# Optimization experiments

Measured on AMD Instinct MI355X. Metric: run time of the kernel, lower is better.

The kernel has to match this reference:

```python
import jax, jax.numpy as jnp
import numpy as np

B, CIN, D, H, W = 2, 64, 16, 16, 16
CK, CV, COUT = 32, 64, 64
EPS = 1e-5


def setup_inputs() -> dict:
    key = jax.random.key(0)
    ks = jax.random.split(key, 11)
    return {
        "x": jax.random.normal(ks[0], (B, CIN, D, H, W), jnp.float32),
        "key_w": jax.random.normal(ks[1], (CK, CIN), jnp.float32) * 0.1,
        "bn_gamma": jax.random.uniform(ks[2], (CK,), jnp.float32, 0.5, 1.5),
        "bn_beta": jax.random.normal(ks[3], (CK,), jnp.float32) * 0.1,
        "bn_mean": jax.random.normal(ks[4], (CK,), jnp.float32) * 0.1,
        "bn_var": jax.random.uniform(ks[5], (CK,), jnp.float32, 0.5, 1.5),
        "value_w": jax.random.normal(ks[6], (CV, CIN), jnp.float32) * 0.1,
        "value_b": jax.random.normal(ks[7], (CV,), jnp.float32) * 0.1,
        "W_w": jax.random.normal(ks[8], (COUT, CV), jnp.float32) * 0.1,
        "W_b": jax.random.normal(ks[9], (COUT,), jnp.float32) * 0.1,
        "gamma": jax.random.normal(ks[10], (1,), jnp.float32),
    }


def reference(x, key_w, bn_gamma, bn_beta, bn_mean, bn_var,
              value_w, value_b, W_w, W_b, gamma):
    b, c, d, h, w = x.shape
    n = d * h * w
    xf = x.reshape(b, c, n)                       # [B, Cin, N]
    # f_key: 1x1x1 conv (no bias) + BatchNorm3d (eval mode, running stats)
    k = jnp.einsum('oc,bcn->bon', key_w, xf)      # [B, Ck, N]
    scale_bn = bn_gamma / jnp.sqrt(bn_var + EPS)
    k = (k - bn_mean[:, None]) * scale_bn[:, None] + bn_beta[:, None]
    # key_query_same=True -> query == key (same weights, same input)
    # f_value: 1x1x1 conv with bias
    v = jnp.einsum('oc,bcn->bon', value_w, xf) + value_b[:, None]  # [B, Cv, N]
    # sim_map = Q^T K scaled, softmax over last axis
    sim = jnp.einsum('bkn,bkm->bnm', k, k) * (CK ** -0.5)          # [B, N, N]
    sim = jax.nn.softmax(sim, axis=-1)
    # context = sim @ V^T  -> [B, N, Cv] -> [B, Cv, N]
    ctx = jnp.einsum('bnm,bvm->bvn', sim, v)
    # W: 1x1x1 conv
    ctx = jnp.einsum('ov,bvn->bon', W_w, ctx) + W_b[:, None]       # [B, Cout, N]
    ctx = ctx.reshape(b, COUT, d, h, w)
    # out_add=True branch: gamma * context + x
    return gamma.reshape(()) * ctx + x
```

## Files before the change

### kernel.cpp

```cpp
#include <hip/hip_runtime.h>
#include <hip/hip_bf16.h>
#include <math.h>

#define BATCH 2
#define CIN 64
#define NSP 4096
#define CK 32
#define CV 64
#define COUT 64
#define EPS 1e-5f
#define S4L 0.5050097680523077f

#define KB 64
#define NW 8
#define KPW (NSP / NW)
#define NCH (KPW / KB)

typedef unsigned short ushort_t;
using bf16x8 = __attribute__((ext_vector_type(8))) short;
using bf16x4 = __attribute__((ext_vector_type(4))) short;
using f32x4  = __attribute__((ext_vector_type(4))) float;
using float4_t = __attribute__((ext_vector_type(4))) float;

__device__ inline ushort_t f2bf(float f) {
  __hip_bfloat16 h = __float2bfloat16(f);
  return *reinterpret_cast<ushort_t*>(&h);
}

__global__ __launch_bounds__(256) void kv_kernel(
    const float* __restrict__ x,
    const float* __restrict__ key_w,
    const float* __restrict__ bn_gamma,
    const float* __restrict__ bn_beta,
    const float* __restrict__ bn_mean,
    const float* __restrict__ bn_var,
    const float* __restrict__ value_w,
    const float* __restrict__ value_b,
    ushort_t* __restrict__ KbT,
    ushort_t* __restrict__ Vbf) {
  __shared__ ushort_t XL[32][66];

  int tid = threadIdx.x, wid = tid >> 6, lane = tid & 63;
  int l15 = lane & 15, g = lane >> 4;
  int b  = blockIdx.x / (NSP / 32);
  int n0 = (blockIdx.x % (NSP / 32)) * 32;

  {
    int n = tid & 31, c8 = tid >> 5;
    const float* xb = x + ((size_t)b * CIN + c8 * 8) * NSP + n0 + n;
#pragma unroll
    for (int j = 0; j < 8; ++j)
      XL[n][c8 * 8 + j] = f2bf(xb[(size_t)j * NSP]);
  }
  __syncthreads();

  if (wid < 2) {
    bf16x8 a[2];
#pragma unroll
    for (int kk = 0; kk < 2; ++kk)
      a[kk] = *(const bf16x8*)&XL[wid * 16 + l15][kk * 32 + g * 8];
#pragma unroll
    for (int osub = 0; osub < 2; ++osub) {
      bf16x8 bb[2];
#pragma unroll
      for (int kk = 0; kk < 2; ++kk) {
        const float* wp = key_w + (osub * 16 + l15) * CIN + kk * 32 + g * 8;
#pragma unroll
        for (int j = 0; j < 8; ++j) bb[kk][j] = (short)f2bf(wp[j]);
      }
      f32x4 d = {0.f, 0.f, 0.f, 0.f};
      d = __builtin_amdgcn_mfma_f32_16x16x32_bf16(a[0], bb[0], d, 0, 0, 0);
      d = __builtin_amdgcn_mfma_f32_16x16x32_bf16(a[1], bb[1], d, 0, 0, 0);
      int o = osub * 16 + l15;
      float sc  = bn_gamma[o] * rsqrtf(bn_var[o] + EPS);
      float scl = sc * S4L;
      float bi  = (bn_beta[o] - bn_mean[o] * sc) * S4L;
#pragma unroll
      for (int r = 0; r < 4; ++r) {
        int n = n0 + wid * 16 + 4 * g + r;
        KbT[((size_t)b * NSP + n) * CK + o] = f2bf(d[r] * scl + bi);
      }
    }
  } else {
    bf16x8 bbv[2][2];
#pragma unroll
    for (int nsub = 0; nsub < 2; ++nsub)
#pragma unroll
      for (int kk = 0; kk < 2; ++kk)
        bbv[nsub][kk] = *(const bf16x8*)&XL[nsub * 16 + l15][kk * 32 + g * 8];
#pragma unroll
    for (int os = 0; os < 2; ++os) {
      int osub = (wid - 2) * 2 + os;
      bf16x8 av[2];
#pragma unroll
      for (int kk = 0; kk < 2; ++kk) {
        const float* wp = value_w + (osub * 16 + l15) * CIN + kk * 32 + g * 8;
#pragma unroll
        for (int j = 0; j < 8; ++j) av[kk][j] = (short)f2bf(wp[j]);
      }
#pragma unroll
      for (int nsub = 0; nsub < 2; ++nsub) {
        f32x4 d = {0.f, 0.f, 0.f, 0.f};
        d = __builtin_amdgcn_mfma_f32_16x16x32_bf16(av[0], bbv[nsub][0], d, 0, 0, 0);
        d = __builtin_amdgcn_mfma_f32_16x16x32_bf16(av[1], bbv[nsub][1], d, 0, 0, 0);
#pragma unroll
        for (int r = 0; r < 4; ++r) {
          int o = osub * 16 + 4 * g + r;
          int n = n0 + nsub * 16 + l15;
          Vbf[((size_t)b * CV + o) * NSP + n] = f2bf(d[r] + value_b[o]);
        }
      }
    }
  }
}

__global__ __launch_bounds__(512) void attn_proj_kernel(
    const ushort_t* __restrict__ KbT,
    const ushort_t* __restrict__ Vbf,
    const float* __restrict__ Ww,
    const float* __restrict__ Wb,
    const float* __restrict__ gamma,
    const float* __restrict__ x,
    float* __restrict__ out) {
  __shared__ __align__(16) ushort_t SMEM[NW * 8192];

  int tid = threadIdx.x, wid = tid >> 6, lane = tid & 63;
  int l15 = lane & 15, g = lane >> 4;
  int b  = blockIdx.x / (NSP / 32);
  int q0 = (blockIdx.x % (NSP / 32)) * 32;

  const ushort_t* Kb = KbT + (size_t)b * NSP * CK;
  const ushort_t* Vb = Vbf + (size_t)b * CV * NSP;

  bf16x8 qf[2];
#pragma unroll
  for (int qg = 0; qg < 2; ++qg)
    qf[qg] = *(const bf16x8*)&Kb[(size_t)(q0 + qg * 16 + l15) * CK + g * 8];
  asm volatile("s_waitcnt vmcnt(0)" ::: "memory");
  __builtin_amdgcn_sched_barrier(0);

  f32x4 acc[2][4];
  float Ssum[2] = {0.f, 0.f};
#pragma unroll
  for (int qg = 0; qg < 2; ++qg)
#pragma unroll
    for (int cg = 0; cg < 4; ++cg)
#pragma unroll
      for (int r = 0; r < 4; ++r) acc[qg][cg][r] = 0.f;

  int kbase = wid * KPW;

  auto stageK = [&](int buf, int n0k) {
    ushort_t* dstb = &SMEM[wid * 8192 + buf * 2048];
#pragma unroll
    for (int i = 0; i < 4; ++i) {
      int off = i * 1024 + lane * 16;
      int key = off >> 6;
      int c16 = (off >> 4) & 3;
      int sw  = c16 ^ ((key >> 1) & 3);
      const ushort_t* src = Kb + (size_t)(n0k + key) * CK + sw * 8;
      __builtin_amdgcn_global_load_lds(
          (const __attribute__((address_space(1))) unsigned int*)src,
          (__attribute__((address_space(3))) unsigned int*)&dstb[i * 512], 16, 0, 0);
    }
  };
  auto stageV = [&](int n0k) {
    ushort_t* dstb = &SMEM[wid * 8192 + 4096];
#pragma unroll
    for (int i = 0; i < 8; ++i) {
      int off = i * 1024 + lane * 16;
      int cv  = off >> 7;
      int c16 = (off >> 4) & 7;
      int sw  = c16 ^ (cv & 7);
      const ushort_t* src = Vb + (size_t)cv * NSP + n0k + sw * 8;
      __builtin_amdgcn_global_load_lds(
          (const __attribute__((address_space(1))) unsigned int*)src,
          (__attribute__((address_space(3))) unsigned int*)&dstb[i * 512], 16, 0, 0);
    }
  };

  stageK(0, kbase);
  stageV(kbase);
  stageK(1, kbase + KB);
  asm volatile("s_waitcnt vmcnt(12)" ::: "memory");
  __builtin_amdgcn_sched_barrier(0);

#pragma unroll
  for (int t = 0; t < NCH; ++t) {
    const ushort_t* KTc = &SMEM[wid * 8192 + (t & 1) * 2048];
    const ushort_t* VTc = &SMEM[wid * 8192 + 4096];

    bf16x8 kf[4];
#pragma unroll
    for (int kg = 0; kg < 4; ++kg) {
      int key = kg * 16 + l15;
      int sw  = g ^ ((key >> 1) & 3);
      kf[kg] = *(const bf16x8*)&KTc[key * CK + sw * 8];
    }
    f32x4 s[2][4];
#pragma unroll
    for (int qg = 0; qg < 2; ++qg)
#pragma unroll
      for (int kg = 0; kg < 4; ++kg) {
        f32x4 z = {0.f, 0.f, 0.f, 0.f};
        s[qg][kg] = __builtin_amdgcn_mfma_f32_16x16x32_bf16(kf[kg], qf[qg], z, 0, 0, 0);
      }

    float p[2][4][4];
#pragma unroll
    for (int qg = 0; qg < 2; ++qg)
#pragma unroll
      for (int kg = 0; kg < 4; ++kg) {
        float ps = 0.f;
#pragma unroll
        for (int r = 0; r < 4; ++r) {
          p[qg][kg][r] = exp2f(s[qg][kg][r]);
          ps += p[qg][kg][r];
        }
        Ssum[qg] += ps;
      }
    bf16x8 pa[2][2];
#pragma unroll
    for (int ks = 0; ks < 2; ++ks)
#pragma unroll
      for (int qg = 0; qg < 2; ++qg)
#pragma unroll
        for (int j = 0; j < 4; ++j) {
          pa[ks][qg][j]     = (short)f2bf(p[qg][2 * ks][j]);
          pa[ks][qg][4 + j] = (short)f2bf(p[qg][2 * ks + 1][j]);
        }

    if (t < NCH - 1) asm volatile("s_waitcnt vmcnt(4)" ::: "memory");
    else             asm volatile("s_waitcnt vmcnt(0)" ::: "memory");
    __builtin_amdgcn_sched_barrier(0);

#pragma unroll
    for (int ks = 0; ks < 2; ++ks) {
#pragma unroll
      for (int cg = 0; cg < 4; ++cg) {
        int cv   = cg * 16 + l15;
        int x7   = cv & 7;
        int half = (g & 1) * 4;
        int t0   = (4 * ks + (g >> 1)) ^ x7;
        int t1   = (4 * ks + 2 + (g >> 1)) ^ x7;
        const ushort_t* vrow = &VTc[cv * KB];
        bf16x4 lo = *(const bf16x4*)&vrow[t0 * 8 + half];
        bf16x4 hi = *(const bf16x4*)&vrow[t1 * 8 + half];
        bf16x8 vf;
#pragma unroll
        for (int j = 0; j < 4; ++j) { vf[j] = lo[j]; vf[4 + j] = hi[j]; }
#pragma unroll
        for (int qg = 0; qg < 2; ++qg)
          acc[qg][cg] = __builtin_amdgcn_mfma_f32_16x16x32_bf16(pa[ks][qg], vf, acc[qg][cg], 0, 0, 0);
      }
    }

    asm volatile("s_waitcnt lgkmcnt(0)" ::: "memory");
    __builtin_amdgcn_sched_barrier(0);

    if (t + 1 < NCH) stageV(kbase + (t + 1) * KB);
    if (t + 2 < NCH) stageK(t & 1, kbase + (t + 2) * KB);

    if (t + 2 < NCH)      asm volatile("s_waitcnt vmcnt(12)" ::: "memory");
    else if (t + 1 < NCH) asm volatile("s_waitcnt vmcnt(8)" ::: "memory");
    __builtin_amdgcn_sched_barrier(0);
  }

#pragma unroll
  for (int qg = 0; qg < 2; ++qg) {
    Ssum[qg] += __shfl_xor(Ssum[qg], 16, 64);
    Ssum[qg] += __shfl_xor(Ssum[qg], 32, 64);
  }

  __syncthreads();
  float* red = (float*)&SMEM[0];
  float* SsR = red + NW * 32 * 68;
#pragma unroll
  for (int qg = 0; qg < 2; ++qg) {
#pragma unroll
    for (int cg = 0; cg < 4; ++cg)
#pragma unroll
      for (int r = 0; r < 4; ++r) {
        int ql = qg * 16 + 4 * g + r;
        red[(wid * 32 + ql) * 68 + cg * 16 + l15] = acc[qg][cg][r];
      }
    if (g == 0) SsR[wid * 32 + qg * 16 + l15] = Ssum[qg];
  }
  __syncthreads();

  int n  = tid & 31;
  int og = tid >> 5;
  float ds = 0.f;
#pragma unroll
  for (int w = 0; w < NW; ++w) ds += SsR[w * 32 + n];
  float invn = 1.f / ds;

  const float4_t* Ww4 = (const float4_t*)Ww;
  float pacc[4];
#pragma unroll
  for (int j = 0; j < 4; ++j) pacc[j] = 0.f;
#pragma unroll
  for (int v4 = 0; v4 < 16; ++v4) {
    float4_t c4 = {0.f, 0.f, 0.f, 0.f};
#pragma unroll
    for (int w = 0; w < NW; ++w) {
      float4_t t4 = *(const float4_t*)&red[(w * 32 + n) * 68 + v4 * 4];
      c4[0] += t4[0]; c4[1] += t4[1]; c4[2] += t4[2]; c4[3] += t4[3];
    }
#pragma unroll
    for (int j = 0; j < 4; ++j) {
      float4_t w4 = Ww4[(og * 4 + j) * 16 + v4];
      pacc[j] += w4[0] * c4[0] + w4[1] * c4[1] + w4[2] * c4[2] + w4[3] * c4[3];
    }
  }

  float gma = gamma[0];
#pragma unroll
  for (int j = 0; j < 4; ++j) {
    int o = og * 4 + j;
    size_t oi = ((size_t)b * COUT + o) * NSP + q0 + n;
    out[oi] = gma * (pacc[j] * invn + Wb[o]) + x[oi];
  }
}

extern "C" void kernel_launch(void* const* d_in, const int* in_sizes, int n_in,
                              void* d_out, int out_size, void* d_ws, size_t ws_size,
                              hipStream_t stream) {
  const float* x        = (const float*)d_in[0];
  const float* key_w    = (const float*)d_in[1];
  const float* bn_gamma = (const float*)d_in[2];
  const float* bn_beta  = (const float*)d_in[3];
  const float* bn_mean  = (const float*)d_in[4];
  const float* bn_var   = (const float*)d_in[5];
  const float* value_w  = (const float*)d_in[6];
  const float* value_b  = (const float*)d_in[7];
  const float* W_w      = (const float*)d_in[8];
  const float* W_b      = (const float*)d_in[9];
  const float* gamma    = (const float*)d_in[10];
  float* out = (float*)d_out;

  ushort_t* KbT = (ushort_t*)d_ws;
  ushort_t* Vbf = KbT + (size_t)BATCH * NSP * CK;

  kv_kernel<<<BATCH * (NSP / 32), 256, 0, stream>>>(
      x, key_w, bn_gamma, bn_beta, bn_mean, bn_var, value_w, value_b, KbT, Vbf);
  attn_proj_kernel<<<BATCH * (NSP / 32), 512, 0, stream>>>(
      KbT, Vbf, W_w, W_b, gamma, x, out);
}
```

Measured before the change: 30.40 us.

## Split key range across 16 waves with smaller chunks and two-level reduction

The attention kernel now runs 1024 threads (16 waves) per 32-query block instead of 8 waves, and halves the key chunk size to 32 so per-wave LDS stays the same in total. The cross-wave reduction becomes two-stage: the upper 8 waves write partials, the lower 8 add and rewrite them, and the final projection then gives each thread 2 output channels. The aim is more latency hiding and shorter per-wave serial loops. The cost is less work per async load, a smaller MFMA batch per chunk, and an extra barrier in the reduction.

```diff
diff --git a/kernel.cpp b/kernel.cpp
--- a/kernel.cpp
+++ b/kernel.cpp
@@ -11,8 +11,8 @@
 #define EPS 1e-5f
 #define S4L 0.5050097680523077f
 
-#define KB 64
-#define NW 8
+#define KB 32
+#define NW 16
 #define KPW (NSP / NW)
 #define NCH (KPW / KB)
 
@@ -114,7 +114,7 @@
   }
 }
 
-__global__ __launch_bounds__(512) void attn_proj_kernel(
+__global__ __launch_bounds__(1024, 4) void attn_proj_kernel(
     const ushort_t* __restrict__ KbT,
     const ushort_t* __restrict__ Vbf,
     const float* __restrict__ Ww,
@@ -122,7 +122,7 @@
     const float* __restrict__ gamma,
     const float* __restrict__ x,
     float* __restrict__ out) {
-  __shared__ __align__(16) ushort_t SMEM[NW * 8192];
+  __shared__ __align__(16) ushort_t SMEM[NW * 4096];
 
   int tid = threadIdx.x, wid = tid >> 6, lane = tid & 63;
   int l15 = lane & 15, g = lane >> 4;
@@ -151,9 +151,9 @@
   int kbase = wid * KPW;
 
   auto stageK = [&](int buf, int n0k) {
-    ushort_t* dstb = &SMEM[wid * 8192 + buf * 2048];
-#pragma unroll
-    for (int i = 0; i < 4; ++i) {
+    ushort_t* dstb = &SMEM[wid * 4096 + buf * 1024];
+#pragma unroll
+    for (int i = 0; i < 2; ++i) {
       int off = i * 1024 + lane * 16;
       int key = off >> 6;
       int c16 = (off >> 4) & 3;
@@ -165,13 +165,13 @@
     }
   };
   auto stageV = [&](int n0k) {
-    ushort_t* dstb = &SMEM[wid * 8192 + 4096];
-#pragma unroll
-    for (int i = 0; i < 8; ++i) {
+    ushort_t* dstb = &SMEM[wid * 4096 + 2048];
+#pragma unroll
+    for (int i = 0; i < 4; ++i) {
       int off = i * 1024 + lane * 16;
-      int cv  = off >> 7;
-      int c16 = (off >> 4) & 7;
-      int sw  = c16 ^ (cv & 7);
+      int cv  = off >> 6;
+      int c16 = (off >> 4) & 3;
+      int sw  = c16 ^ (cv & 3);
       const ushort_t* src = Vb + (size_t)cv * NSP + n0k + sw * 8;
       __builtin_amdgcn_global_load_lds(
           (const __attribute__((address_space(1))) unsigned int*)src,
@@ -182,35 +182,35 @@
   stageK(0, kbase);
   stageV(kbase);
   stageK(1, kbase + KB);
-  asm volatile("s_waitcnt vmcnt(12)" ::: "memory");
+  asm volatile("s_waitcnt vmcnt(6)" ::: "memory");
   __builtin_amdgcn_sched_barrier(0);
 
 #pragma unroll
   for (int t = 0; t < NCH; ++t) {
-    const ushort_t* KTc = &SMEM[wid * 8192 + (t & 1) * 2048];
-    const ushort_t* VTc = &SMEM[wid * 8192 + 4096];
-
-    bf16x8 kf[4];
-#pragma unroll
-    for (int kg = 0; kg < 4; ++kg) {
+    const ushort_t* KTc = &SMEM[wid * 4096 + (t & 1) * 1024];
+    const ushort_t* VTc = &SMEM[wid * 4096 + 2048];
+
+    bf16x8 kf[2];
+#pragma unroll
+    for (int kg = 0; kg < 2; ++kg) {
       int key = kg * 16 + l15;
       int sw  = g ^ ((key >> 1) & 3);
       kf[kg] = *(const bf16x8*)&KTc[key * CK + sw * 8];
     }
-    f32x4 s[2][4];
+    f32x4 s[2][2];
 #pragma unroll
     for (int qg = 0; qg < 2; ++qg)
 #pragma unroll
-      for (int kg = 0; kg < 4; ++kg) {
+      for (int kg = 0; kg < 2; ++kg) {
         f32x4 z = {0.f, 0.f, 0.f, 0.f};
         s[qg][kg] = __builtin_amdgcn_mfma_f32_16x16x32_bf16(kf[kg], qf[qg], z, 0, 0, 0);
       }
 
-    float p[2][4][4];
+    float p[2][2][4];
 #pragma unroll
     for (int qg = 0; qg < 2; ++qg)
 #pragma unroll
-      for (int kg = 0; kg < 4; ++kg) {
+      for (int kg = 0; kg < 2; ++kg) {
         float ps = 0.f;
 #pragma unroll
         for (int r = 0; r < 4; ++r) {
@@ -219,40 +219,35 @@
         }
         Ssum[qg] += ps;
       }
-    bf16x8 pa[2][2];
-#pragma unroll
-    for (int ks = 0; ks < 2; ++ks)
-#pragma unroll
-      for (int qg = 0; qg < 2; ++qg)
-#pragma unroll
-        for (int j = 0; j < 4; ++j) {
-          pa[ks][qg][j]     = (short)f2bf(p[qg][2 * ks][j]);
-          pa[ks][qg][4 + j] = (short)f2bf(p[qg][2 * ks + 1][j]);
-        }
-
-    if (t < NCH - 1) asm volatile("s_waitcnt vmcnt(4)" ::: "memory");
+    bf16x8 pa[2];
+#pragma unroll
+    for (int qg = 0; qg < 2; ++qg)
+#pragma unroll
+      for (int j = 0; j < 4; ++j) {
+        pa[qg][j]     = (short)f2bf(p[qg][0][j]);
+        pa[qg][4 + j] = (short)f2bf(p[qg][1][j]);
+      }
+
+    if (t < NCH - 1) asm volatile("s_waitcnt vmcnt(2)" ::: "memory");
     else             asm volatile("s_waitcnt vmcnt(0)" ::: "memory");
     __builtin_amdgcn_sched_barrier(0);
 
 #pragma unroll
-    for (int ks = 0; ks < 2; ++ks) {
-#pragma unroll
-      for (int cg = 0; cg < 4; ++cg) {
-        int cv   = cg * 16 + l15;
-        int x7   = cv & 7;
-        int half = (g & 1) * 4;
-        int t0   = (4 * ks + (g >> 1)) ^ x7;
-        int t1   = (4 * ks + 2 + (g >> 1)) ^ x7;
-        const ushort_t* vrow = &VTc[cv * KB];
-        bf16x4 lo = *(const bf16x4*)&vrow[t0 * 8 + half];
-        bf16x4 hi = *(const bf16x4*)&vrow[t1 * 8 + half];
-        bf16x8 vf;
-#pragma unroll
-        for (int j = 0; j < 4; ++j) { vf[j] = lo[j]; vf[4 + j] = hi[j]; }
-#pragma unroll
-        for (int qg = 0; qg < 2; ++qg)
-          acc[qg][cg] = __builtin_amdgcn_mfma_f32_16x16x32_bf16(pa[ks][qg], vf, acc[qg][cg], 0, 0, 0);
-      }
+    for (int cg = 0; cg < 4; ++cg) {
+      int cv   = cg * 16 + l15;
+      int x3   = cv & 3;
+      int half = (g & 1) * 4;
+      int t0   = (g >> 1) ^ x3;
+      int t1   = (2 + (g >> 1)) ^ x3;
+      const ushort_t* vrow = &VTc[cv * KB];
+      bf16x4 lo = *(const bf16x4*)&vrow[t0 * 8 + half];
+      bf16x4 hi = *(const bf16x4*)&vrow[t1 * 8 + half];
+      bf16x8 vf;
+#pragma unroll
+      for (int j = 0; j < 4; ++j) { vf[j] = lo[j]; vf[4 + j] = hi[j]; }
+#pragma unroll
+      for (int qg = 0; qg < 2; ++qg)
+        acc[qg][cg] = __builtin_amdgcn_mfma_f32_16x16x32_bf16(pa[qg], vf, acc[qg][cg], 0, 0, 0);
     }
 
     asm volatile("s_waitcnt lgkmcnt(0)" ::: "memory");
@@ -261,8 +256,8 @@
     if (t + 1 < NCH) stageV(kbase + (t + 1) * KB);
     if (t + 2 < NCH) stageK(t & 1, kbase + (t + 2) * KB);
 
-    if (t + 2 < NCH)      asm volatile("s_waitcnt vmcnt(12)" ::: "memory");
-    else if (t + 1 < NCH) asm volatile("s_waitcnt vmcnt(8)" ::: "memory");
+    if (t + 2 < NCH)      asm volatile("s_waitcnt vmcnt(6)" ::: "memory");
+    else if (t + 1 < NCH) asm volatile("s_waitcnt vmcnt(4)" ::: "memory");
     __builtin_amdgcn_sched_barrier(0);
   }
 
@@ -274,17 +269,46 @@
 
   __syncthreads();
   float* red = (float*)&SMEM[0];
-  float* SsR = red + NW * 32 * 68;
-#pragma unroll
-  for (int qg = 0; qg < 2; ++qg) {
-#pragma unroll
-    for (int cg = 0; cg < 4; ++cg)
-#pragma unroll
-      for (int r = 0; r < 4; ++r) {
-        int ql = qg * 16 + 4 * g + r;
-        red[(wid * 32 + ql) * 68 + cg * 16 + l15] = acc[qg][cg][r];
-      }
-    if (g == 0) SsR[wid * 32 + qg * 16 + l15] = Ssum[qg];
+  float* SsR = red + 8 * 32 * 68;
+
+  if (wid >= 8) {
+    int w = wid - 8;
+#pragma unroll
+    for (int qg = 0; qg < 2; ++qg) {
+#pragma unroll
+      for (int cg = 0; cg < 4; ++cg)
+#pragma unroll
+        for (int r = 0; r < 4; ++r) {
+          int ql = qg * 16 + 4 * g + r;
+          red[(w * 32 + ql) * 68 + cg * 16 + l15] = acc[qg][cg][r];
+        }
+      if (g == 0) SsR[w * 32 + qg * 16 + l15] = Ssum[qg];
+    }
+  }
+  __syncthreads();
+  if (wid < 8) {
+#pragma unroll
+    for (int qg = 0; qg < 2; ++qg) {
+#pragma unroll
+      for (int cg = 0; cg < 4; ++cg)
+#pragma unroll
+        for (int r = 0; r < 4; ++r) {
+          int ql = qg * 16 + 4 * g + r;
+          acc[qg][cg][r] += red[(wid * 32 + ql) * 68 + cg * 16 + l15];
+        }
+      Ssum[qg] += SsR[wid * 32 + qg * 16 + l15];
+    }
+#pragma unroll
+    for (int qg = 0; qg < 2; ++qg) {
+#pragma unroll
+      for (int cg = 0; cg < 4; ++cg)
+#pragma unroll
+        for (int r = 0; r < 4; ++r) {
+          int ql = qg * 16 + 4 * g + r;
+          red[(wid * 32 + ql) * 68 + cg * 16 + l15] = acc[qg][cg][r];
+        }
+      if (g == 0) SsR[wid * 32 + qg * 16 + l15] = Ssum[qg];
+    }
   }
   __syncthreads();
 
@@ -292,32 +316,31 @@
   int og = tid >> 5;
   float ds = 0.f;
 #pragma unroll
-  for (int w = 0; w < NW; ++w) ds += SsR[w * 32 + n];
+  for (int w = 0; w < 8; ++w) ds += SsR[w * 32 + n];
   float invn = 1.f / ds;
 
   const float4_t* Ww4 = (const float4_t*)Ww;
-  float pacc[4];
-#pragma unroll
-  for (int j = 0; j < 4; ++j) pacc[j] = 0.f;
+  float pacc[2];
+  pacc[0] = 0.f; pacc[1] = 0.f;
 #pragma unroll
   for (int v4 = 0; v4 < 16; ++v4) {
     float4_t c4 = {0.f, 0.f, 0.f, 0.f};
 #pragma unroll
-    for (int w = 0; w < NW; ++w) {
+    for (int w = 0; w < 8; ++w) {
       float4_t t4 = *(const float4_t*)&red[(w * 32 + n) * 68 + v4 * 4];
       c4[0] += t4[0]; c4[1] += t4[1]; c4[2] += t4[2]; c4[3] += t4[3];
     }
 #pragma unroll
-    for (int j = 0; j < 4; ++j) {
-      float4_t w4 = Ww4[(og * 4 + j) * 16 + v4];
+    for (int j = 0; j < 2; ++j) {
+      float4_t w4 = Ww4[(og * 2 + j) * 16 + v4];
       pacc[j] += w4[0] * c4[0] + w4[1] * c4[1] + w4[2] * c4[2] + w4[3] * c4[3];
     }
   }
 
   float gma = gamma[0];
 #pragma unroll
-  for (int j = 0; j < 4; ++j) {
-    int o = og * 4 + j;
+  for (int j = 0; j < 2; ++j) {
+    int o = og * 2 + j;
     size_t oi = ((size_t)b * COUT + o) * NSP + q0 + n;
     out[oi] = gma * (pacc[j] * invn + Wb[o]) + x[oi];
   }
@@ -344,6 +367,6 @@
 
   kv_kernel<<<BATCH * (NSP / 32), 256, 0, stream>>>(
       x, key_w, bn_gamma, bn_beta, bn_mean, bn_var, value_w, value_b, KbT, Vbf);
-  attn_proj_kernel<<<BATCH * (NSP / 32), 512, 0, stream>>>(
+  attn_proj_kernel<<<BATCH * (NSP / 32), 1024, 0, stream>>>(
       KbT, Vbf, W_w, W_b, gamma, x, out);
 }
```

Result: slower. 31.15 us (+2.4%).
